# Kernel tuning notes

Hardware: AMD Instinct MI355X
Metric: run time of the kernel (lower is better)

## Reference

```python
import jax, jax.numpy as jnp
import numpy as np


def _maxpool3d(x, s=2):
    # MaxPool3d(kernel_size=s) -> stride=s, VALID padding
    return jax.lax.reduce_window(x, -jnp.inf, jax.lax.max,
                                 (1, 1, s, s, s), (1, 1, s, s, s), 'VALID')


def _spectral_norm(W, u):
    # W: [out_c, in_c]. One power iteration with u/v detached, matching
    # torch.nn.utils.spectral_norm's training-step behavior.
    v = W.T @ u
    v = v / (jnp.linalg.norm(v) + 1e-12)
    u2 = W @ v
    u2 = u2 / (jnp.linalg.norm(u2) + 1e-12)
    u2 = jax.lax.stop_gradient(u2)
    v = jax.lax.stop_gradient(v)
    sigma = u2 @ (W @ v)
    return W / sigma


def setup_inputs() -> dict:
    key = jax.random.key(0)
    ks = jax.random.split(key, 6)
    B, C, D = 4, 256, 32
    kc, vc, oc = 128, 128, 256
    return {
        'x':  jax.random.normal(ks[0], (B, C, D, D, D), jnp.float32),
        'Wk': jax.random.normal(ks[1], (kc, C), jnp.float32) * 0.05,  # shared f_key/f_query 1x1x1 conv
        'bk': jnp.zeros((kc,), jnp.float32),
        'Wv': jax.random.normal(ks[2], (vc, C), jnp.float32) * 0.05,  # f_value 1x1x1 conv
        'bv': jnp.zeros((vc,), jnp.float32),
        'Ww': jax.random.normal(ks[3], (oc, vc), jnp.float32) * 0.05,  # output W 1x1x1 conv
        'bw': jnp.zeros((oc,), jnp.float32),
        'u':  jax.random.normal(ks[4], (kc,), jnp.float32),            # spectral-norm power-iter vector
    }


def reference(x, Wk, bk, Wv, bv, Ww, bw, u):
    B, C = x.shape[0], x.shape[1]
    kc = Wk.shape[0]
    xp = _maxpool3d(x, 2)                      # [B,C,16,16,16]
    sp = xp.shape[2:]
    N = sp[0] * sp[1] * sp[2]                  # 4096 flattened positions
    xf = xp.reshape(B, C, N)                   # [B,C,N]

    Wq = _spectral_norm(Wk, u)                 # f_query = f_key (shared weights)
    q = jnp.einsum('kc,bcn->bnk', Wq, xf) + bk                    # [B,N,kc]
    k = jnp.einsum('kc,bcn->bkn', Wq, xf) + bk[None, :, None]     # [B,kc,N]
    v = jnp.einsum('vc,bcn->bnv', Wv, xf) + bv                    # [B,N,vc]

    sim = jnp.einsum('bnk,bkm->bnm', q, k) * (kc ** -0.5)         # [B,N,N]
    attn = jax.nn.softmax(sim, axis=-1)
    ctx = jnp.einsum('bnm,bmv->bnv', attn, v)                     # [B,N,vc]

    out = jnp.einsum('ov,bnv->bon', Ww, ctx) + bw[None, :, None]  # [B,oc,N]
    return out.reshape(B, Ww.shape[0], *sp)    # [B,oc,16,16,16] (pooled spatial, as in original)
```

## Files before the change

### kernel.cpp

```cpp
#include <hip/hip_runtime.h>

typedef __attribute__((ext_vector_type(8))) short short8;
typedef __attribute__((ext_vector_type(4))) float f32x4;
typedef __attribute__((ext_vector_type(16))) float f32x16;

static constexpr size_t OFF_SIGMA = 0;
static constexpr size_t OFF_ML    = 256;
static constexpr size_t OFF_QKT   = 1048576;
static constexpr size_t OFF_V     = OFF_QKT + 4194304;
static constexpr size_t OFF_WCAT  = OFF_V + 4194304;
static constexpr size_t OFF_PC    = OFF_WCAT + 196608;

__device__ inline unsigned short f2bf(float f) {
  unsigned int u = __float_as_uint(f);
  unsigned int r = u + 0x7fffu + ((u >> 16) & 1u);
  return (unsigned short)(r >> 16);
}
__device__ inline float bf2f(unsigned short s) {
  return __uint_as_float(((unsigned int)s) << 16);
}
__device__ inline unsigned int cvtpk_bf16(float a, float b) {
  unsigned int r;
  asm("v_cvt_pk_bf16_f32 %0, %1, %2" : "=v"(r) : "v"(a), "v"(b));
  return r;
}

__launch_bounds__(256)
__global__ void k_init(const float* __restrict__ Ww, const float* __restrict__ Wk,
                       const float* __restrict__ Wv, const float* __restrict__ u,
                       unsigned short* __restrict__ wcat, float* __restrict__ sig) {
  __shared__ float WT[256][129];
  __shared__ float red[256];
  __shared__ float vsh[256];
  __shared__ float ush[128];
  int t = threadIdx.x;
  if (blockIdx.x < 96) {
    int i = (blockIdx.x * 256 + t) * 4;
    const float* src = (i < 32768) ? (Ww + i) : (i < 65536) ? (Wk + i - 32768)
                                                            : (Wv + i - 65536);
    float4 w = *(const float4*)src;
    unsigned int lo = (unsigned int)f2bf(w.x) | ((unsigned int)f2bf(w.y) << 16);
    unsigned int hi = (unsigned int)f2bf(w.z) | ((unsigned int)f2bf(w.w) << 16);
    *(uint2*)(wcat + i) = make_uint2(lo, hi);
    return;
  }
#pragma unroll
  for (int i = 0; i < 32; i++) {
    int idx = i * 1024 + t * 4;
    float4 w = *(const float4*)(Wk + idx);
    int k = idx >> 8, c = idx & 255;
    WT[c][k] = w.x; WT[c + 1][k] = w.y; WT[c + 2][k] = w.z; WT[c + 3][k] = w.w;
  }
  if (t < 128) ush[t] = u[t];
  __syncthreads();
  float acc = 0.f;
#pragma unroll 8
  for (int k = 0; k < 128; k++) acc += WT[t][k] * ush[k];
  vsh[t] = acc;
  red[t] = acc * acc;
  __syncthreads();
  for (int s = 128; s > 0; s >>= 1) { if (t < s) red[t] += red[t + s]; __syncthreads(); }
  float nrm = sqrtf(red[0]) + 1e-12f;
  float vn = vsh[t] / nrm;
  __syncthreads();
  vsh[t] = vn;
  __syncthreads();
  float acc2 = 0.f;
  if (t < 128) {
#pragma unroll 8
    for (int c = 0; c < 256; c++) acc2 += WT[c][t] * vsh[c];
  }
  red[t] = (t < 128) ? acc2 * acc2 : 0.f;
  __syncthreads();
  for (int s = 128; s > 0; s >>= 1) { if (t < s) red[t] += red[t + s]; __syncthreads(); }
  if (t == 0) {
    float s2v = red[0];
    sig[0] = s2v / (sqrtf(s2v) + 1e-12f);
  }
}

__launch_bounds__(256)
__global__ void k_qkv(const float* __restrict__ x,
                      const unsigned short* __restrict__ wcat,
                      const float* __restrict__ bk, const float* __restrict__ bv,
                      const float* __restrict__ sig,
                      unsigned short* __restrict__ qkT, unsigned short* __restrict__ vws) {
  __shared__ __align__(16) unsigned short Bl[64 * 64];
  int bid = blockIdx.x;
  int nt = bid & 63, b = bid >> 6;
  int n0 = nt * 64;
  int t = threadIdx.x, wid = t >> 6, lane = t & 63, g = lane >> 4, lr = lane & 15;
  int R0 = wid * 64;
  bool isq = (wid < 2);
  const unsigned short* wb = isq ? (wcat + 32768 + (size_t)R0 * 256)
                                 : (wcat + 65536 + (size_t)(R0 - 128) * 256);
  f32x4 acc[4][4];
#pragma unroll
  for (int i = 0; i < 4; i++)
#pragma unroll
    for (int j = 0; j < 4; j++) acc[i][j] = (f32x4){0.f, 0.f, 0.f, 0.f};

  int cc = t >> 2, q4 = t & 3;
  int d0p = n0 >> 8;
  int d1p = ((n0 >> 4) & 15) + q4;
  const float* xrow = x + ((size_t)(b * 256) << 15) + d0p * 2048 + d1p * 64;

  unsigned short pool[16];
#define POOLLOAD(C)                                                          \
  {                                                                          \
    const float* pr_ = xrow + (size_t)(C) * 32768;                           \
    _Pragma("unroll")                                                        \
    for (int k8 = 0; k8 < 8; k8++) {                                         \
      float4 a_ = *(const float4*)(pr_ + k8 * 4);                            \
      float4 b_ = *(const float4*)(pr_ + 32 + k8 * 4);                       \
      float4 c_ = *(const float4*)(pr_ + 1024 + k8 * 4);                     \
      float4 d_ = *(const float4*)(pr_ + 1056 + k8 * 4);                     \
      float p0_ = fmaxf(fmaxf(fmaxf(a_.x, a_.y), fmaxf(b_.x, b_.y)),         \
                        fmaxf(fmaxf(c_.x, c_.y), fmaxf(d_.x, d_.y)));        \
      float p1_ = fmaxf(fmaxf(fmaxf(a_.z, a_.w), fmaxf(b_.z, b_.w)),         \
                        fmaxf(fmaxf(c_.z, c_.w), fmaxf(d_.z, d_.w)));        \
      pool[k8 * 2] = f2bf(p0_);                                              \
      pool[k8 * 2 + 1] = f2bf(p1_);                                          \
    }                                                                        \
  }

  POOLLOAD(cc)

#pragma unroll 1
  for (int ks4 = 0; ks4 < 4; ks4++) {
    int k0 = ks4 * 64;
    __syncthreads();
#pragma unroll
    for (int j = 0; j < 16; j++) {
      int nn = q4 * 16 + j;
      Bl[nn * 64 + (((cc >> 3) ^ (nn & 7)) << 3) + (cc & 7)] = pool[j];
    }
    if (ks4 < 3) POOLLOAD(k0 + 64 + cc)
    __syncthreads();
#pragma unroll
    for (int ks2 = 0; ks2 < 2; ks2++) {
      short8 af[4], bf[4];
#pragma unroll
      for (int ot = 0; ot < 4; ot++)
        af[ot] = *(const short8*)(wb + (size_t)(ot * 16 + lr) * 256 + k0 + ks2 * 32 + g * 8);
#pragma unroll
      for (int nt2 = 0; nt2 < 4; nt2++) {
        int n = nt2 * 16 + lr;
        bf[nt2] = *(const short8*)(Bl + n * 64 + (((ks2 * 4 + g) ^ (n & 7)) << 3));
      }
#pragma unroll
      for (int ot = 0; ot < 4; ot++)
#pragma unroll
        for (int nt2 = 0; nt2 < 4; nt2++)
          acc[ot][nt2] = __builtin_amdgcn_mfma_f32_16x16x32_bf16(af[ot], bf[nt2],
                                                                 acc[ot][nt2], 0, 0, 0);
    }
  }
#undef POOLLOAD

  if (isq) {
    float inv_s = 1.0f / sig[0];
#pragma unroll
    for (int ot = 0; ot < 4; ot++)
#pragma unroll
      for (int rr = 0; rr < 4; rr++) {
        int d = R0 + ot * 16 + g * 4 + rr;
        float bias = bk[d];
#pragma unroll
        for (int nt2 = 0; nt2 < 4; nt2++) {
          int n = n0 + nt2 * 16 + lr;
          float val = acc[ot][nt2][rr] * inv_s + bias;
          int ds = ((((d >> 3) ^ (n & 7)) & 15) << 3) | (d & 7);
          qkT[((size_t)b * 4096 + n) * 128 + ds] = f2bf(val);
        }
      }
  } else {
#pragma unroll
    for (int ot = 0; ot < 4; ot++)
#pragma unroll
      for (int rr = 0; rr < 4; rr++) {
        int d = R0 - 128 + ot * 16 + g * 4 + rr;
        float bias = bv[d];
#pragma unroll
        for (int nt2 = 0; nt2 < 4; nt2++) {
          int n = n0 + nt2 * 16 + lr;
          int c = n & 63;
          int cs = ((((c >> 3) ^ (d & 7)) & 7) << 3) | (c & 7);
          vws[((size_t)(b * 128 + d)) * 4096 + (n & ~63) + cs] =
              f2bf(acc[ot][nt2][rr] + bias);
        }
      }
  }
}

__launch_bounds__(256, 2)
__global__ void k_attn(const unsigned short* __restrict__ qkT,
                       const unsigned short* __restrict__ vws,
                       unsigned short* __restrict__ pc, float* __restrict__ lsum) {
  __shared__ __align__(16) char smem[2][32768];
  const float C1 = 0.12751744f;
  int p = blockIdx.x;
  int bid = (p & 7) * 64 + (p >> 3);
  int sp = bid & 3, qt = (bid >> 2) & 31, b = bid >> 7;
  int kv0 = sp * 1024;
  int t = threadIdx.x, wid = t >> 6, lane = t & 63;
  int l31 = lane & 31, hi = lane >> 5;
  int qrb = qt * 128 + wid * 32;
  const unsigned short* qk_b = qkT + (size_t)b * 524288;
  const char* kgb = (const char*)qk_b;
  const char* vgb = (const char*)(vws + (size_t)b * 524288);

  bool stk = (wid < 2);
  int ch0 = (wid & 1) * 8;
  const char* vsrc_base = vgb + (size_t)(lane >> 3) * 8192 + (lane & 7) * 16;

#define STAGE(BUF, MB)                                                         \
  {                                                                            \
    char* base_ = smem[BUF];                                                   \
    _Pragma("unroll")                                                          \
    for (int i_ = 0; i_ < 8; i_++) {                                           \
      int ch_ = ch0 + i_;                                                      \
      if (stk) {                                                               \
        const char* g_ = kgb + (size_t)(MB) * 256 + ch_ * 1024 + lane * 16;    \
        __builtin_amdgcn_global_load_lds(                                      \
            (const __attribute__((address_space(1))) unsigned int*)g_,         \
            (__attribute__((address_space(3))) unsigned int*)(base_ + ch_ * 1024), \
            16, 0, 0);                                                         \
      } else {                                                                 \
        const char* g_ = vsrc_base + (size_t)ch_ * 65536 + (size_t)(MB) * 2;   \
        __builtin_amdgcn_global_load_lds(                                      \
            (const __attribute__((address_space(1))) unsigned int*)g_,         \
            (__attribute__((address_space(3))) unsigned int*)(base_ + 16384 + ch_ * 1024), \
            16, 0, 0);                                                         \
      }                                                                        \
    }                                                                          \
  }

  STAGE(0, kv0)

  short8 qf[8];
  {
    int row = qrb + l31;
    const unsigned short* qr = qk_b + (size_t)row * 128;
#pragma unroll
    for (int kk = 0; kk < 8; kk++)
      qf[kk] = *(const short8*)(qr + (((2 * kk + hi) ^ (row & 7)) << 3));
  }

  f32x16 acc[4];
#pragma unroll
  for (int dt = 0; dt < 4; dt++)
#pragma unroll
    for (int r = 0; r < 16; r++) acc[dt][r] = 0.f;
  float lacc = 0.f;

  __syncthreads();

#pragma unroll 1
  for (int it = 0; it < 16; ++it) {
    int cur = it & 1;
    if (it < 15) STAGE(cur ^ 1, kv0 + it * 64 + 64)
    const char* KL = smem[cur];
    const char* VL = smem[cur] + 16384;

    f32x16 s0, s1;
#pragma unroll
    for (int r = 0; r < 16; r++) { s0[r] = 0.f; s1[r] = 0.f; }
    __builtin_amdgcn_s_setprio(1);
#pragma unroll
    for (int kk = 0; kk < 8; kk++) {
      int cs = 2 * kk + hi;
      short8 kf0 = *(const short8*)(KL + l31 * 256 + ((cs ^ (l31 & 7)) << 4));
      short8 kf1 = *(const short8*)(KL + (32 + l31) * 256 + ((cs ^ (l31 & 7)) << 4));
      s0 = __builtin_amdgcn_mfma_f32_32x32x16_bf16(kf0, qf[kk], s0, 0, 0, 0);
      s1 = __builtin_amdgcn_mfma_f32_32x32x16_bf16(kf1, qf[kk], s1, 0, 0, 0);
    }
    __builtin_amdgcn_s_setprio(0);

    short8 pa[4];
#pragma unroll
    for (int ct = 0; ct < 2; ct++) {
      unsigned int w0[4], w1[4];
#pragma unroll
      for (int a = 0; a < 4; a++) {
        float v0 = ct ? s1[4 * a + 0] : s0[4 * a + 0];
        float v1 = ct ? s1[4 * a + 1] : s0[4 * a + 1];
        float v2 = ct ? s1[4 * a + 2] : s0[4 * a + 2];
        float v3 = ct ? s1[4 * a + 3] : s0[4 * a + 3];
        float p0 = __builtin_amdgcn_exp2f(v0 * C1);
        float p1 = __builtin_amdgcn_exp2f(v1 * C1);
        float p2 = __builtin_amdgcn_exp2f(v2 * C1);
        float p3 = __builtin_amdgcn_exp2f(v3 * C1);
        lacc += (p0 + p1) + (p2 + p3);
        w0[a] = cvtpk_bf16(p0, p1);
        w1[a] = cvtpk_bf16(p2, p3);
      }
#pragma unroll
      for (int k2 = 0; k2 < 2; k2++) {
        unsigned int xa = w0[2 * k2], ya = w0[2 * k2 + 1];
        unsigned int xb = w1[2 * k2], yb = w1[2 * k2 + 1];
        asm("v_permlane32_swap_b32 %0, %1" : "+v"(xa), "+v"(ya));
        asm("v_permlane32_swap_b32 %0, %1" : "+v"(xb), "+v"(yb));
        union { unsigned int u[4]; short8 s8; } pk_;
        pk_.u[0] = xa; pk_.u[1] = xb; pk_.u[2] = ya; pk_.u[3] = yb;
        pa[ct * 2 + k2] = pk_.s8;
      }
    }

    __builtin_amdgcn_s_setprio(1);
#pragma unroll
    for (int ks = 0; ks < 4; ks++) {
      int cv = 2 * ks + hi;
#pragma unroll
      for (int dt = 0; dt < 4; dt++) {
        int d = dt * 32 + l31;
        short8 vb = *(const short8*)(VL + d * 128 + ((cv ^ (d & 7)) << 4));
        acc[dt] = __builtin_amdgcn_mfma_f32_32x32x16_bf16(pa[ks], vb, acc[dt], 0, 0, 0);
      }
    }
    __builtin_amdgcn_s_setprio(0);
    __syncthreads();
  }

  float lf = lacc + __shfl_xor(lacc, 32);

  char* OL = smem[0] + wid * 8704;
#pragma unroll
  for (int dt = 0; dt < 4; dt++)
#pragma unroll
    for (int r = 0; r < 16; r++) {
      int q = (r & 3) + 8 * (r >> 2) + 4 * hi;
      *(unsigned short*)(OL + q * 272 + (dt * 32 + l31) * 2) = f2bf(acc[dt][r]);
    }
  unsigned short* dst = pc + ((size_t)sp * 16384 + (size_t)b * 4096 + qrb) * 128;
#pragma unroll
  for (int j = 0; j < 8; j++) {
    int row = lane >> 1;
    int off = (lane & 1) * 128 + j * 16;
    short8 v = *(const short8*)(OL + row * 272 + off);
    *(short8*)((char*)dst + row * 256 + off) = v;
  }
  if (lane < 32) lsum[sp * 16384 + (size_t)b * 4096 + qrb + l31] = lf;
#undef STAGE
}

__launch_bounds__(256)
__global__ void k_mergeout(const unsigned short* __restrict__ pc,
                           const float* __restrict__ lsum,
                           const unsigned short* __restrict__ wwb,
                           const float* __restrict__ bw,
                           float* __restrict__ out) {
  __shared__ float inv_l[64];
  __shared__ __align__(16) unsigned short Bl[64 * 128];
  int bid = blockIdx.x;
  int nt = bid & 63, b = bid >> 6;
  int n0 = nt * 64;
  size_t gnb = (size_t)b * 4096 + n0;
  int t = threadIdx.x;

  if (t < 64) {
    float L = 0.f;
#pragma unroll
    for (int sp = 0; sp < 4; sp++) L += lsum[sp * 16384 + gnb + t];
    inv_l[t] = 1.f / L;
  }
  __syncthreads();

  {
    int n = t & 63, vs = t >> 6;
    float o[32] = {};
#pragma unroll
    for (int sp = 0; sp < 4; sp++) {
      const unsigned short* src = pc + ((size_t)sp * 16384 + gnb + n) * 128 + vs * 32;
#pragma unroll
      for (int c = 0; c < 4; c++) {
        short8 pv = *(const short8*)(src + c * 8);
#pragma unroll
        for (int j = 0; j < 8; j++) o[c * 8 + j] += bf2f((unsigned short)pv[j]);
      }
    }
    float inv = inv_l[n];
    unsigned int* B32 = (unsigned int*)Bl;
#pragma unroll
    for (int jj = 0; jj < 16; jj++) {
      int v = vs * 32 + jj * 2;
      int kg = v >> 3;
      int kgp = (kg & 8) | ((kg ^ n) & 7);
      unsigned int pk = (unsigned int)f2bf(o[jj * 2] * inv) |
                        ((unsigned int)f2bf(o[jj * 2 + 1] * inv) << 16);
      B32[n * 64 + kgp * 4 + ((v & 7) >> 1)] = pk;
    }
  }
  __syncthreads();

  int wid = t >> 6, lane = t & 63, g = lane >> 4, lr = lane & 15;
  int o0 = wid * 64;
  short8 af[4][4];
#pragma unroll
  for (int ot = 0; ot < 4; ot++) {
    int o = o0 + ot * 16 + lr;
#pragma unroll
    for (int ks = 0; ks < 4; ks++)
      af[ot][ks] = *(const short8*)(wwb + (size_t)o * 128 + ks * 32 + g * 8);
  }
  f32x4 acc[4][4];
#pragma unroll
  for (int i = 0; i < 4; i++)
#pragma unroll
    for (int j = 0; j < 4; j++) acc[i][j] = (f32x4){0.f, 0.f, 0.f, 0.f};
#pragma unroll
  for (int nt2 = 0; nt2 < 4; nt2++) {
    short8 bfr[4];
#pragma unroll
    for (int ks = 0; ks < 4; ks++) {
      int kg = ks * 4 + g;
      int kgp = (kg & 8) | ((kg ^ lr) & 7);
      bfr[ks] = *(const short8*)(Bl + (nt2 * 16 + lr) * 128 + kgp * 8);
    }
#pragma unroll
    for (int ot = 0; ot < 4; ot++)
#pragma unroll
      for (int ks = 0; ks < 4; ks++)
        acc[ot][nt2] = __builtin_amdgcn_mfma_f32_16x16x32_bf16(af[ot][ks], bfr[ks],
                                                               acc[ot][nt2], 0, 0, 0);
  }
#pragma unroll
  for (int ot = 0; ot < 4; ot++)
#pragma unroll
    for (int r = 0; r < 4; r++) {
      int o = o0 + ot * 16 + g * 4 + r;
      float bias = bw[o];
#pragma unroll
      for (int nt2 = 0; nt2 < 4; nt2++)
        out[((size_t)(b * 256 + o)) * 4096 + n0 + nt2 * 16 + lr] = acc[ot][nt2][r] + bias;
    }
}

extern "C" void kernel_launch(void* const* d_in, const int* in_sizes, int n_in,
                              void* d_out, int out_size, void* d_ws, size_t ws_size,
                              hipStream_t stream) {
  const float* x  = (const float*)d_in[0];
  const float* Wk = (const float*)d_in[1];
  const float* bk = (const float*)d_in[2];
  const float* Wv = (const float*)d_in[3];
  const float* bv = (const float*)d_in[4];
  const float* Ww = (const float*)d_in[5];
  const float* bw = (const float*)d_in[6];
  const float* u  = (const float*)d_in[7];

  char* ws = (char*)d_ws;
  float* sig            = (float*)(ws + OFF_SIGMA);
  float* lsum           = (float*)(ws + OFF_ML);
  unsigned short* qkT   = (unsigned short*)(ws + OFF_QKT);
  unsigned short* vbuf  = (unsigned short*)(ws + OFF_V);
  unsigned short* wcat  = (unsigned short*)(ws + OFF_WCAT);
  unsigned short* pc    = (unsigned short*)(ws + OFF_PC);
  float* out            = (float*)d_out;

  k_init<<<97, 256, 0, stream>>>(Ww, Wk, Wv, u, wcat, sig);
  k_qkv<<<256, 256, 0, stream>>>(x, wcat, bk, bv, sig, qkT, vbuf);
  k_attn<<<512, 256, 0, stream>>>(qkT, vbuf, pc, lsum);
  k_mergeout<<<256, 256, 0, stream>>>(pc, lsum, wcat, bw, out);
}
```

Before: 101.0 us.

## Fold softmax scale into Q, widen QKV blocks, precompute LDS offsets in attention

The softmax scale constant is now folded into Q during the QKV projection, with sqrt of the log2-scaled factor applied to Q and bias. That removes a multiply per score in the attention inner loop. The QKV kernel moves to 512 threads with half the output rows and half the pooling work per wave, for more parallelism in the pooling loads. The attention loop is unrolled by two with constant buffer indices and precomputed swizzled LDS offsets, to cut address arithmetic. Folding the scale into Q before bf16 rounding slightly changes numerics.

```diff
diff --git a/kernel.cpp b/kernel.cpp
--- a/kernel.cpp
+++ b/kernel.cpp
@@ -79,38 +79,39 @@
   }
 }
 
-__launch_bounds__(256)
+__launch_bounds__(512)
 __global__ void k_qkv(const float* __restrict__ x,
                       const unsigned short* __restrict__ wcat,
                       const float* __restrict__ bk, const float* __restrict__ bv,
                       const float* __restrict__ sig,
                       unsigned short* __restrict__ qkT, unsigned short* __restrict__ vws) {
   __shared__ __align__(16) unsigned short Bl[64 * 64];
+  const float SQC1 = 0.35709584f;
   int bid = blockIdx.x;
   int nt = bid & 63, b = bid >> 6;
   int n0 = nt * 64;
   int t = threadIdx.x, wid = t >> 6, lane = t & 63, g = lane >> 4, lr = lane & 15;
-  int R0 = wid * 64;
-  bool isq = (wid < 2);
+  int R0 = wid * 32;
+  bool isq = (wid < 4);
   const unsigned short* wb = isq ? (wcat + 32768 + (size_t)R0 * 256)
                                  : (wcat + 65536 + (size_t)(R0 - 128) * 256);
-  f32x4 acc[4][4];
-#pragma unroll
-  for (int i = 0; i < 4; i++)
+  f32x4 acc[2][4];
+#pragma unroll
+  for (int i = 0; i < 2; i++)
 #pragma unroll
     for (int j = 0; j < 4; j++) acc[i][j] = (f32x4){0.f, 0.f, 0.f, 0.f};
 
-  int cc = t >> 2, q4 = t & 3;
+  int kh = t & 1, q4 = (t >> 1) & 3, cc = t >> 3;
   int d0p = n0 >> 8;
   int d1p = ((n0 >> 4) & 15) + q4;
-  const float* xrow = x + ((size_t)(b * 256) << 15) + d0p * 2048 + d1p * 64;
-
-  unsigned short pool[16];
+  const float* xrow = x + ((size_t)(b * 256) << 15) + d0p * 2048 + d1p * 64 + kh * 16;
+
+  unsigned short pool[8];
 #define POOLLOAD(C)                                                          \
   {                                                                          \
     const float* pr_ = xrow + (size_t)(C) * 32768;                           \
     _Pragma("unroll")                                                        \
-    for (int k8 = 0; k8 < 8; k8++) {                                         \
+    for (int k8 = 0; k8 < 4; k8++) {                                         \
       float4 a_ = *(const float4*)(pr_ + k8 * 4);                            \
       float4 b_ = *(const float4*)(pr_ + 32 + k8 * 4);                       \
       float4 c_ = *(const float4*)(pr_ + 1024 + k8 * 4);                     \
@@ -131,17 +132,17 @@
     int k0 = ks4 * 64;
     __syncthreads();
 #pragma unroll
-    for (int j = 0; j < 16; j++) {
-      int nn = q4 * 16 + j;
+    for (int j = 0; j < 8; j++) {
+      int nn = q4 * 16 + kh * 8 + j;
       Bl[nn * 64 + (((cc >> 3) ^ (nn & 7)) << 3) + (cc & 7)] = pool[j];
     }
     if (ks4 < 3) POOLLOAD(k0 + 64 + cc)
     __syncthreads();
 #pragma unroll
     for (int ks2 = 0; ks2 < 2; ks2++) {
-      short8 af[4], bf[4];
-#pragma unroll
-      for (int ot = 0; ot < 4; ot++)
+      short8 af[2], bf[4];
+#pragma unroll
+      for (int ot = 0; ot < 2; ot++)
         af[ot] = *(const short8*)(wb + (size_t)(ot * 16 + lr) * 256 + k0 + ks2 * 32 + g * 8);
 #pragma unroll
       for (int nt2 = 0; nt2 < 4; nt2++) {
@@ -149,7 +150,7 @@
         bf[nt2] = *(const short8*)(Bl + n * 64 + (((ks2 * 4 + g) ^ (n & 7)) << 3));
       }
 #pragma unroll
-      for (int ot = 0; ot < 4; ot++)
+      for (int ot = 0; ot < 2; ot++)
 #pragma unroll
         for (int nt2 = 0; nt2 < 4; nt2++)
           acc[ot][nt2] = __builtin_amdgcn_mfma_f32_16x16x32_bf16(af[ot], bf[nt2],
@@ -159,24 +160,24 @@
 #undef POOLLOAD
 
   if (isq) {
-    float inv_s = 1.0f / sig[0];
-#pragma unroll
-    for (int ot = 0; ot < 4; ot++)
+    float s1c = SQC1 / sig[0];
+#pragma unroll
+    for (int ot = 0; ot < 2; ot++)
 #pragma unroll
       for (int rr = 0; rr < 4; rr++) {
         int d = R0 + ot * 16 + g * 4 + rr;
-        float bias = bk[d];
+        float bias = bk[d] * SQC1;
 #pragma unroll
         for (int nt2 = 0; nt2 < 4; nt2++) {
           int n = n0 + nt2 * 16 + lr;
-          float val = acc[ot][nt2][rr] * inv_s + bias;
+          float val = acc[ot][nt2][rr] * s1c + bias;
           int ds = ((((d >> 3) ^ (n & 7)) & 15) << 3) | (d & 7);
           qkT[((size_t)b * 4096 + n) * 128 + ds] = f2bf(val);
         }
       }
   } else {
 #pragma unroll
-    for (int ot = 0; ot < 4; ot++)
+    for (int ot = 0; ot < 2; ot++)
 #pragma unroll
       for (int rr = 0; rr < 4; rr++) {
         int d = R0 - 128 + ot * 16 + g * 4 + rr;
@@ -198,17 +199,17 @@
                        const unsigned short* __restrict__ vws,
                        unsigned short* __restrict__ pc, float* __restrict__ lsum) {
   __shared__ __align__(16) char smem[2][32768];
-  const float C1 = 0.12751744f;
   int p = blockIdx.x;
   int bid = (p & 7) * 64 + (p >> 3);
   int sp = bid & 3, qt = (bid >> 2) & 31, b = bid >> 7;
   int kv0 = sp * 1024;
   int t = threadIdx.x, wid = t >> 6, lane = t & 63;
-  int l31 = lane & 31, hi = lane >> 5;
+  int l31 = lane & 31, hi = lane >> 5, e = l31 & 7;
   int qrb = qt * 128 + wid * 32;
   const unsigned short* qk_b = qkT + (size_t)b * 524288;
   const char* kgb = (const char*)qk_b;
   const char* vgb = (const char*)(vws + (size_t)b * 524288);
+  const char* sbase = smem[0];
 
   bool stk = (wid < 2);
   int ch0 = (wid & 1) * 8;
@@ -247,6 +248,12 @@
       qf[kk] = *(const short8*)(qr + (((2 * kk + hi) ^ (row & 7)) << 3));
   }
 
+  unsigned qoff[8], pvoff[4];
+#pragma unroll
+  for (int kk = 0; kk < 8; kk++) qoff[kk] = l31 * 256 + (((2 * kk + hi) ^ e) << 4);
+#pragma unroll
+  for (int ks = 0; ks < 4; ks++) pvoff[ks] = l31 * 128 + (((2 * ks + hi) ^ e) << 4);
+
   f32x16 acc[4];
 #pragma unroll
   for (int dt = 0; dt < 4; dt++)
@@ -256,71 +263,68 @@
 
   __syncthreads();
 
+#define ATTN_BODY(CUR, DO_STAGE, MBNEXT)                                       \
+  {                                                                            \
+    if (DO_STAGE) STAGE(CUR ^ 1, MBNEXT)                                       \
+    f32x16 s0, s1;                                                             \
+    _Pragma("unroll")                                                          \
+    for (int r = 0; r < 16; r++) { s0[r] = 0.f; s1[r] = 0.f; }                 \
+    __builtin_amdgcn_s_setprio(1);                                             \
+    _Pragma("unroll")                                                          \
+    for (int kk = 0; kk < 8; kk++) {                                           \
+      short8 kf0 = *(const short8*)(sbase + (CUR) * 32768 + qoff[kk]);         \
+      short8 kf1 = *(const short8*)(sbase + (CUR) * 32768 + 8192 + qoff[kk]);  \
+      s0 = __builtin_amdgcn_mfma_f32_32x32x16_bf16(kf0, qf[kk], s0, 0, 0, 0);  \
+      s1 = __builtin_amdgcn_mfma_f32_32x32x16_bf16(kf1, qf[kk], s1, 0, 0, 0);  \
+    }                                                                          \
+    __builtin_amdgcn_s_setprio(0);                                             \
+    short8 pa[4];                                                              \
+    _Pragma("unroll")                                                          \
+    for (int ct = 0; ct < 2; ct++) {                                           \
+      unsigned int w0[4], w1[4];                                               \
+      _Pragma("unroll")                                                        \
+      for (int a = 0; a < 4; a++) {                                            \
+        float p0 = __builtin_amdgcn_exp2f(ct ? s1[4 * a + 0] : s0[4 * a + 0]); \
+        float p1 = __builtin_amdgcn_exp2f(ct ? s1[4 * a + 1] : s0[4 * a + 1]); \
+        float p2 = __builtin_amdgcn_exp2f(ct ? s1[4 * a + 2] : s0[4 * a + 2]); \
+        float p3 = __builtin_amdgcn_exp2f(ct ? s1[4 * a + 3] : s0[4 * a + 3]); \
+        lacc += (p0 + p1) + (p2 + p3);                                         \
+        w0[a] = cvtpk_bf16(p0, p1);                                            \
+        w1[a] = cvtpk_bf16(p2, p3);                                            \
+      }                                                                        \
+      _Pragma("unroll")                                                        \
+      for (int k2 = 0; k2 < 2; k2++) {                                         \
+        unsigned int xa = w0[2 * k2], ya = w0[2 * k2 + 1];                     \
+        unsigned int xb = w1[2 * k2], yb = w1[2 * k2 + 1];                     \
+        asm("v_permlane32_swap_b32 %0, %1" : "+v"(xa), "+v"(ya));              \
+        asm("v_permlane32_swap_b32 %0, %1" : "+v"(xb), "+v"(yb));              \
+        union { unsigned int u[4]; short8 s8; } pk_;                           \
+        pk_.u[0] = xa; pk_.u[1] = xb; pk_.u[2] = ya; pk_.u[3] = yb;            \
+        pa[ct * 2 + k2] = pk_.s8;                                              \
+      }                                                                        \
+    }                                                                          \
+    __builtin_amdgcn_s_setprio(1);                                             \
+    _Pragma("unroll")                                                          \
+    for (int ks = 0; ks < 4; ks++) {                                           \
+      _Pragma("unroll")                                                        \
+      for (int dt = 0; dt < 4; dt++) {                                         \
+        short8 vb = *(const short8*)(sbase + (CUR) * 32768 + 16384 +           \
+                                     dt * 4096 + pvoff[ks]);                   \
+        acc[dt] = __builtin_amdgcn_mfma_f32_32x32x16_bf16(pa[ks], vb, acc[dt], \
+                                                          0, 0, 0);            \
+      }                                                                        \
+    }                                                                          \
+    __builtin_amdgcn_s_setprio(0);                                             \
+    __syncthreads();                                                           \
+  }
+
 #pragma unroll 1
-  for (int it = 0; it < 16; ++it) {
-    int cur = it & 1;
-    if (it < 15) STAGE(cur ^ 1, kv0 + it * 64 + 64)
-    const char* KL = smem[cur];
-    const char* VL = smem[cur] + 16384;
-
-    f32x16 s0, s1;
-#pragma unroll
-    for (int r = 0; r < 16; r++) { s0[r] = 0.f; s1[r] = 0.f; }
-    __builtin_amdgcn_s_setprio(1);
-#pragma unroll
-    for (int kk = 0; kk < 8; kk++) {
-      int cs = 2 * kk + hi;
-      short8 kf0 = *(const short8*)(KL + l31 * 256 + ((cs ^ (l31 & 7)) << 4));
-      short8 kf1 = *(const short8*)(KL + (32 + l31) * 256 + ((cs ^ (l31 & 7)) << 4));
-      s0 = __builtin_amdgcn_mfma_f32_32x32x16_bf16(kf0, qf[kk], s0, 0, 0, 0);
-      s1 = __builtin_amdgcn_mfma_f32_32x32x16_bf16(kf1, qf[kk], s1, 0, 0, 0);
-    }
-    __builtin_amdgcn_s_setprio(0);
-
-    short8 pa[4];
-#pragma unroll
-    for (int ct = 0; ct < 2; ct++) {
-      unsigned int w0[4], w1[4];
-#pragma unroll
-      for (int a = 0; a < 4; a++) {
-        float v0 = ct ? s1[4 * a + 0] : s0[4 * a + 0];
-        float v1 = ct ? s1[4 * a + 1] : s0[4 * a + 1];
-        float v2 = ct ? s1[4 * a + 2] : s0[4 * a + 2];
-        float v3 = ct ? s1[4 * a + 3] : s0[4 * a + 3];
-        float p0 = __builtin_amdgcn_exp2f(v0 * C1);
-        float p1 = __builtin_amdgcn_exp2f(v1 * C1);
-        float p2 = __builtin_amdgcn_exp2f(v2 * C1);
-        float p3 = __builtin_amdgcn_exp2f(v3 * C1);
-        lacc += (p0 + p1) + (p2 + p3);
-        w0[a] = cvtpk_bf16(p0, p1);
-        w1[a] = cvtpk_bf16(p2, p3);
-      }
-#pragma unroll
-      for (int k2 = 0; k2 < 2; k2++) {
-        unsigned int xa = w0[2 * k2], ya = w0[2 * k2 + 1];
-        unsigned int xb = w1[2 * k2], yb = w1[2 * k2 + 1];
-        asm("v_permlane32_swap_b32 %0, %1" : "+v"(xa), "+v"(ya));
-        asm("v_permlane32_swap_b32 %0, %1" : "+v"(xb), "+v"(yb));
-        union { unsigned int u[4]; short8 s8; } pk_;
-        pk_.u[0] = xa; pk_.u[1] = xb; pk_.u[2] = ya; pk_.u[3] = yb;
-        pa[ct * 2 + k2] = pk_.s8;
-      }
-    }
-
-    __builtin_amdgcn_s_setprio(1);
-#pragma unroll
-    for (int ks = 0; ks < 4; ks++) {
-      int cv = 2 * ks + hi;
-#pragma unroll
-      for (int dt = 0; dt < 4; dt++) {
-        int d = dt * 32 + l31;
-        short8 vb = *(const short8*)(VL + d * 128 + ((cv ^ (d & 7)) << 4));
-        acc[dt] = __builtin_amdgcn_mfma_f32_32x32x16_bf16(pa[ks], vb, acc[dt], 0, 0, 0);
-      }
-    }
-    __builtin_amdgcn_s_setprio(0);
-    __syncthreads();
-  }
+  for (int it2 = 0; it2 < 8; ++it2) {
+    int mb0 = kv0 + it2 * 128;
+    ATTN_BODY(0, true, mb0 + 64)
+    ATTN_BODY(1, (it2 < 7), mb0 + 128)
+  }
+#undef ATTN_BODY
 
   float lf = lacc + __shfl_xor(lacc, 32);
 
@@ -458,7 +462,7 @@
   float* out            = (float*)d_out;
 
   k_init<<<97, 256, 0, stream>>>(Ww, Wk, Wv, u, wcat, sig);
-  k_qkv<<<256, 256, 0, stream>>>(x, wcat, bk, bv, sig, qkT, vbuf);
+  k_qkv<<<256, 512, 0, stream>>>(x, wcat, bk, bv, sig, qkT, vbuf);
   k_attn<<<512, 256, 0, stream>>>(qkT, vbuf, pc, lsum);
   k_mergeout<<<256, 256, 0, stream>>>(pc, lsum, wcat, bw, out);
 }
```

Result: faster. 92.30 us (-8.6%).
